# Kernel optimization log

Hardware: AMD Instinct MI355X
Metric: run time of the kernel (lower is better)

The kernel has to match this reference:

```python
import jax, jax.numpy as jnp
import numpy as np

C = 256
NUM_HEADS = 4
GROUPS = 8
EPS = 1e-5


def setup_inputs() -> dict:
    key = jax.random.key(0)
    ks = jax.random.split(key, 8)
    N, H, W = 4, 64, 64
    x = jax.random.normal(ks[0], (N, C, H, W), dtype=jnp.float32)
    mask = jnp.ones((N, 1, H, W), dtype=jnp.float32)
    norm_w = jax.random.normal(ks[1], (C,), dtype=jnp.float32) * 0.02 + 1.0
    norm_b = jax.random.normal(ks[2], (C,), dtype=jnp.float32) * 0.02
    qkv_w = jax.random.normal(ks[3], (3 * C, C), dtype=jnp.float32) * (1.0 / np.sqrt(C))
    qkv_b = jax.random.normal(ks[4], (3 * C,), dtype=jnp.float32) * 0.02
    proj_w = jax.random.normal(ks[5], (C, C), dtype=jnp.float32) * (1.0 / np.sqrt(C))
    proj_b = jax.random.normal(ks[6], (C,), dtype=jnp.float32) * 0.02
    return {"x": x, "mask": mask, "norm_w": norm_w, "norm_b": norm_b,
            "qkv_w": qkv_w, "qkv_b": qkv_b, "proj_w": proj_w, "proj_b": proj_b}


def _group_norm(x, w, b):
    # x: [N, C, H, W]; normalize within GROUPS groups over (C//G, H, W)
    N, Cc, H, W = x.shape
    xg = x.reshape(N, GROUPS, Cc // GROUPS, H, W)
    mean = xg.mean(axis=(2, 3, 4), keepdims=True)
    var = xg.var(axis=(2, 3, 4), keepdims=True)
    xg = (xg - mean) * jax.lax.rsqrt(var + EPS)
    x = xg.reshape(N, Cc, H, W)
    return x * w[None, :, None, None] + b[None, :, None, None]


def reference(x, mask, norm_w, norm_b, qkv_w, qkv_b, proj_w, proj_b):
    N, Cc, H, W = x.shape
    h = NUM_HEADS
    hd = Cc // h  # head dim
    x_norm = _group_norm(x, norm_w, norm_b)
    # 1x1 conv == channel matmul: [N, 3C, H, W]
    qkv = jnp.einsum('nchw,oc->nohw', x_norm, qkv_w) + qkv_b[None, :, None, None]
    q, k, v = jnp.split(qkv, 3, axis=1)
    # n (h c) y x -> n h (y x) c
    def to_heads(t):
        return t.reshape(N, h, hd, H * W).transpose(0, 1, 3, 2)
    q, k, v = to_heads(q), to_heads(k), to_heads(v)
    scale = hd ** (-0.5)
    scores = jnp.einsum('nhic,nhjc->nhij', q, k) * scale  # [N,h,HW,HW]
    probs = jax.nn.softmax(scores, axis=-1)
    out = jnp.einsum('nhij,nhjc->nhic', probs, v)  # [N,h,HW,hd]
    # n h (y x) c -> n (h c) y x
    out = out.transpose(0, 1, 3, 2).reshape(N, Cc, H, W)
    out = jnp.einsum('nchw,oc->nohw', out, proj_w) + proj_b[None, :, None, None]
    y = (x + out) * mask[:, :1, :, :]  # broadcast over C (== repeat)
    return (y, mask)
```

## Files before the change

### kernel.cpp

```cpp
#include <hip/hip_runtime.h>

#define HW 4096
#define EPSV 1e-5f
#define SCL (0.125f * 1.44269504088896341f)

typedef unsigned short u16;
typedef unsigned int u32;
typedef __attribute__((ext_vector_type(8))) short short8;
typedef __attribute__((ext_vector_type(4))) short short4v;
typedef __attribute__((ext_vector_type(4))) float f32x4;

#define MFMA_K32(a, b, c) __builtin_amdgcn_mfma_f32_16x16x32_bf16((a), (b), (c), 0, 0, 0)
#if __has_builtin(__builtin_amdgcn_mfma_f32_16x16x16bf16_1k)
#define MFMA_K16(a, b, c) __builtin_amdgcn_mfma_f32_16x16x16bf16_1k((a), (b), (c), 0, 0, 0)
#elif __has_builtin(__builtin_amdgcn_mfma_f32_16x16x16_bf16)
#define MFMA_K16(a, b, c) __builtin_amdgcn_mfma_f32_16x16x16_bf16((a), (b), (c), 0, 0, 0)
#else
#define MFMA_K16(a, b, c) (c)
#endif

#define GLDS(g, l) __builtin_amdgcn_global_load_lds( \
    (const __attribute__((address_space(1))) u16*)(g), \
    (__attribute__((address_space(3))) u16*)(l), 16, 0, 0)

__device__ __forceinline__ u16 f2b(float f) {
    u32 u = __float_as_uint(f);
    u32 r = (u + 0x7FFFu + ((u >> 16) & 1u)) >> 16;
    return (u16)r;
}

__global__ __launch_bounds__(256) void gn_partial(const float* __restrict__ x, float* __restrict__ ps,
                                                  const float* __restrict__ mask, float* __restrict__ outm) {
    int bid = blockIdx.x;
    int t = threadIdx.x;
    if (bid < 16) {
        ((float4*)outm)[bid * 256 + t] = ((const float4*)mask)[bid * 256 + t];
    }
    const float4* base = (const float4*)x + (size_t)bid * 2048;
    float s = 0.f, sq = 0.f;
    for (int i = t; i < 2048; i += 256) {
        float4 v = base[i];
        s += v.x + v.y + v.z + v.w;
        sq += v.x * v.x + v.y * v.y + v.z * v.z + v.w * v.w;
    }
    __shared__ float rs[256], rq[256];
    rs[t] = s; rq[t] = sq;
    __syncthreads();
    for (int o = 128; o > 0; o >>= 1) {
        if (t < o) { rs[t] += rs[t + o]; rq[t] += rq[t + o]; }
        __syncthreads();
    }
    if (t == 0) { ps[2 * bid] = rs[0]; ps[2 * bid + 1] = rq[0]; }
}

__global__ __launch_bounds__(256) void prep(const float* __restrict__ ps, float* __restrict__ stats,
                                            const float* __restrict__ qkv_w, u16* __restrict__ Wqb,
                                            const float* __restrict__ proj_w, u16* __restrict__ Wpb) {
    int bid = blockIdx.x;
    int t = threadIdx.x;
    if (bid == 0) {
        if (t < 32) {
            float s = 0.f, sq = 0.f;
            for (int i = 0; i < 16; i++) {
                s += ps[2 * (t * 16 + i)];
                sq += ps[2 * (t * 16 + i) + 1];
            }
            float mean = s * (1.f / 131072.f);
            float var = sq * (1.f / 131072.f) - mean * mean;
            stats[t] = mean;
            stats[32 + t] = rsqrtf(var + EPSV);
        }
        return;
    }
    const float* src; u16* dst; int nscaled; int idx;
    if (bid <= 192) { src = qkv_w; dst = Wqb; nscaled = 256; idx = (bid - 1) * 256 + t; }
    else            { src = proj_w; dst = Wpb; nscaled = 0;   idx = (bid - 193) * 256 + t; }
    int row = idx >> 6;
    float sc = (row < nscaled) ? SCL : 1.0f;
    float4 v = *((const float4*)src + idx);
    u32 lo = (u32)f2b(v.x * sc) | ((u32)f2b(v.y * sc) << 16);
    u32 hi = (u32)f2b(v.z * sc) | ((u32)f2b(v.w * sc) << 16);
    uint2 o; o.x = lo; o.y = hi;
    *(uint2*)(dst + (size_t)idx * 4) = o;
}

__global__ __launch_bounds__(256) void gn_apply_t(const float* __restrict__ x, const float* __restrict__ w,
                                                  const float* __restrict__ b, const float* __restrict__ stats,
                                                  u16* __restrict__ xt) {
    __shared__ u16 Tt[64][72];
    int t = threadIdx.x;
    int p0 = blockIdx.x * 64;
    int c0 = blockIdx.y * 64;
    int n = blockIdx.z;
    int pc = (t & 15) * 4;
#pragma unroll
    for (int jj = 0; jj < 4; jj++) {
        int r = (t >> 4) + jj * 16;
        int c = c0 + r;
        int grp = n * 8 + (c >> 5);
        float mean = stats[grp], rstd = stats[32 + grp];
        float a = rstd * w[c];
        float bb = b[c] - mean * a;
        float4 v = *(const float4*)(x + ((size_t)n * 256 + c) * HW + p0 + pc);
        Tt[pc + 0][r] = f2b(v.x * a + bb);
        Tt[pc + 1][r] = f2b(v.y * a + bb);
        Tt[pc + 2][r] = f2b(v.z * a + bb);
        Tt[pc + 3][r] = f2b(v.w * a + bb);
    }
    __syncthreads();
    int p = t >> 2, ck = t & 3;
    short8 s0 = *(const short8*)&Tt[p][ck * 16];
    short8 s1 = *(const short8*)&Tt[p][ck * 16 + 8];
    u16* dst = xt + ((size_t)n * HW + p0 + p) * 256 + c0 + ck * 16;
    *(short8*)dst = s0;
    *(short8*)(dst + 8) = s1;
}

__global__ __launch_bounds__(256) void qkv_mfma(const u16* __restrict__ xt, const u16* __restrict__ Wb,
                                                const float* __restrict__ bq, u16* __restrict__ Qw,
                                                u16* __restrict__ Kw, u16* __restrict__ Vw) {
    __shared__ u16 Xs[64 * 256];
    int t = threadIdx.x;
    int w = t >> 6, lane = t & 63;
    int col = lane & 15, quad = lane >> 4;
    int p0 = blockIdx.x * 64;
    int n = blockIdx.z;

#pragma unroll
    for (int j = 0; j < 8; j++) {
        int rl = j * 2 + (lane >> 5);
        int row = w * 16 + rl;
        int slot = (lane & 31) ^ (rl & 7);
        GLDS(xt + ((size_t)n * HW + p0 + row) * 256 + slot * 8, Xs + (w * 16 + j * 2) * 256);
    }

    const u16* wrow = Wb + (size_t)(w * 16 + col) * 256 + quad * 8;
    short8 A[8];
#pragma unroll
    for (int ks = 0; ks < 8; ks++) A[ks] = *(const short8*)(wrow + ks * 32);

    __syncthreads();

    int c7 = col & 7;
    for (int ot = 0; ot < 12; ot++) {
        int o0 = ot * 64;
        short8 An[8];
        if (ot < 11) {
            const u16* wn = wrow + (size_t)(o0 + 64) * 256;
#pragma unroll
            for (int ks = 0; ks < 8; ks++) An[ks] = *(const short8*)(wn + ks * 32);
        }

        f32x4 C[4];
#pragma unroll
        for (int pb = 0; pb < 4; pb++) C[pb] = (f32x4){0.f, 0.f, 0.f, 0.f};
#pragma unroll
        for (int pb = 0; pb < 4; pb++) {
            const u16* xr = Xs + (pb * 16 + col) * 256;
#pragma unroll
            for (int ks = 0; ks < 8; ks++) {
                int slot = (ks * 4 + quad) ^ c7;
                short8 Bf = *(const short8*)(xr + slot * 8);
                C[pb] = MFMA_K32(A[ks], Bf, C[pb]);
            }
        }

        int type = o0 >> 8;
        int h = (o0 >> 6) & 3;
        int nh = n * 4 + h;
        float sc = (type == 0) ? SCL : 1.0f;
        if (type == 2) {
#pragma unroll
            for (int rg = 0; rg < 4; rg++) {
                int d = w * 16 + quad * 4 + rg;
                float bias = bq[o0 + d];
                u16* vb = Vw + ((size_t)nh * 64 + d) * HW + p0 + col;
#pragma unroll
                for (int pb = 0; pb < 4; pb++)
                    vb[pb * 16] = f2b(C[pb][rg] + bias);
            }
        } else {
            u16* dst = (type == 0 ? Qw : Kw) + ((size_t)nh * HW + p0 + col) * 64 + w * 16 + quad * 4;
            float b0 = sc * bq[o0 + w * 16 + quad * 4 + 0];
            float b1 = sc * bq[o0 + w * 16 + quad * 4 + 1];
            float b2 = sc * bq[o0 + w * 16 + quad * 4 + 2];
            float b3 = sc * bq[o0 + w * 16 + quad * 4 + 3];
#pragma unroll
            for (int pb = 0; pb < 4; pb++) {
                uint2 o;
                o.x = (u32)f2b(C[pb][0] + b0) | ((u32)f2b(C[pb][1] + b1) << 16);
                o.y = (u32)f2b(C[pb][2] + b2) | ((u32)f2b(C[pb][3] + b3) << 16);
                *(uint2*)(dst + (size_t)(pb * 16) * 64) = o;
            }
        }
#pragma unroll
        for (int ks = 0; ks < 8; ks++) A[ks] = An[ks];
    }
}

__global__ __launch_bounds__(512, 4) void flash_mfma(const u16* __restrict__ Qw, const u16* __restrict__ Kw,
                                                     const u16* __restrict__ Vw, u16* __restrict__ attnT) {
    __shared__ u16 Ks[4][64 * 64];
    __shared__ u16 Vts[4][64 * 64];
    int t = threadIdx.x;
    int w = t >> 6, lane = t & 63;
    int half = w >> 2, wl = w & 3;
    int col = lane & 15, quad = lane >> 4;
    int q0 = blockIdx.x * 128;
    int nh = blockIdx.y;

    const u16* qp = Qw + ((size_t)nh * HW + q0 + wl * 32 + col) * 64 + quad * 8;
    short8 qa0 = *(const short8*)qp;
    short8 qa1 = *(const short8*)(qp + 32);
    short8 qc0 = *(const short8*)(qp + 1024);
    short8 qc1 = *(const short8*)(qp + 1024 + 32);

    f32x4 OaA[4], OaB[4];
#pragma unroll
    for (int db = 0; db < 4; db++) {
        OaA[db] = (f32x4){0.f, 0.f, 0.f, 0.f};
        OaB[db] = (f32x4){0.f, 0.f, 0.f, 0.f};
    }
    f32x4 lacA = (f32x4){0.f, 0.f, 0.f, 0.f};
    f32x4 lacB = (f32x4){0.f, 0.f, 0.f, 0.f};

    const u16* kbase = Kw + (size_t)nh * HW * 64;
    const u16* vbase = Vw + (size_t)nh * 64 * HW;
    int lrK = lane >> 3;
    int ccK = lane & 7;
    size_t kSrc = (size_t)(wl * 8 + lrK) * 64 + (ccK ^ lrK) * 8;
    int jbase = half * 2048;

#define STAGE(jt_, b_) do { \
        int j0_ = jbase + (jt_) * 64; \
        _Pragma("unroll") \
        for (int s_ = 0; s_ < 2; s_++) \
            GLDS(kbase + (size_t)j0_ * 64 + kSrc + (size_t)(s_ * 32) * 64, &Ks[half * 2 + (b_)][(wl * 8 + s_ * 32) * 64]); \
        _Pragma("unroll") \
        for (int s_ = 0; s_ < 2; s_++) { \
            int d_ = wl * 8 + s_ * 32 + lrK; \
            GLDS(vbase + (size_t)d_ * HW + j0_ + ((ccK ^ lrK) * 8), &Vts[half * 2 + (b_)][(wl * 8 + s_ * 32) * 64]); \
        } \
    } while (0)

    STAGE(0, 0);
    STAGE(1, 1);

    int c7 = col & 7;
    const short4v ones = {0x3F80, 0x3F80, 0x3F80, 0x3F80};
    for (int jt = 0; jt < 32; jt++) {
        int cur = jt & 1;
        if (jt < 31) { asm volatile("s_waitcnt vmcnt(4)" ::: "memory"); }
        else         { asm volatile("s_waitcnt vmcnt(0)" ::: "memory"); }
        __builtin_amdgcn_s_barrier();

        const u16* KsC = Ks[half * 2 + cur];
        const u16* VtC = Vts[half * 2 + cur];

        f32x4 sA[4], sB[4];
        __builtin_amdgcn_s_setprio(1);
#pragma unroll
        for (int jb = 0; jb < 4; jb++) {
            const u16* kr = KsC + (jb * 16 + col) * 64;
            short8 ka0 = *(const short8*)(kr + ((quad ^ c7) * 8));
            short8 ka1 = *(const short8*)(kr + (((quad + 4) ^ c7) * 8));
            f32x4 a = (f32x4){0.f, 0.f, 0.f, 0.f};
            a = MFMA_K32(ka0, qa0, a);
            a = MFMA_K32(ka1, qa1, a);
            sA[jb] = a;
            f32x4 b = (f32x4){0.f, 0.f, 0.f, 0.f};
            b = MFMA_K32(ka0, qc0, b);
            b = MFMA_K32(ka1, qc1, b);
            sB[jb] = b;
        }
        __builtin_amdgcn_s_setprio(0);

        short4v ptA[4], ptB[4];
#pragma unroll
        for (int jb = 0; jb < 4; jb++) {
            u32 ua[4], ub[4];
#pragma unroll
            for (int rg = 0; rg < 4; rg++) {
                ua[rg] = __float_as_uint(__builtin_amdgcn_exp2f(sA[jb][rg])) + 0x8000u;
                ub[rg] = __float_as_uint(__builtin_amdgcn_exp2f(sB[jb][rg])) + 0x8000u;
            }
            uint2 pa2, pb2;
            pa2.x = __builtin_amdgcn_perm(ua[1], ua[0], 0x07060302u);
            pa2.y = __builtin_amdgcn_perm(ua[3], ua[2], 0x07060302u);
            pb2.x = __builtin_amdgcn_perm(ub[1], ub[0], 0x07060302u);
            pb2.y = __builtin_amdgcn_perm(ub[3], ub[2], 0x07060302u);
            ptA[jb] = __builtin_bit_cast(short4v, pa2);
            ptB[jb] = __builtin_bit_cast(short4v, pb2);
        }

        __builtin_amdgcn_s_setprio(1);
#pragma unroll
        for (int jb = 0; jb < 4; jb++) {
            lacA = MFMA_K16(ones, ptA[jb], lacA);
            lacB = MFMA_K16(ones, ptB[jb], lacB);
        }
#pragma unroll
        for (int db = 0; db < 4; db++) {
            const u16* vr = VtC + (db * 16 + col) * 64;
#pragma unroll
            for (int jb = 0; jb < 4; jb++) {
                int ch = jb * 2 + (quad >> 1);
                short4v va = *(const short4v*)(vr + ((ch ^ c7) * 8) + (quad & 1) * 4);
                OaA[db] = MFMA_K16(va, ptA[jb], OaA[db]);
                OaB[db] = MFMA_K16(va, ptB[jb], OaB[db]);
            }
        }
        __builtin_amdgcn_s_setprio(0);

        __builtin_amdgcn_s_barrier();
        if (jt < 30) STAGE(jt + 2, cur);
    }
#undef STAGE

    float* mO = (float*)&Ks[0][0];
    float* mL = (float*)&Vts[0][0];
    int widx = wl * 64 + lane;
    if (half == 1) {
#pragma unroll
        for (int db = 0; db < 4; db++) {
#pragma unroll
            for (int rg = 0; rg < 4; rg++) {
                mO[(db * 8 + rg) * 256 + widx] = OaA[db][rg];
                mO[(db * 8 + 4 + rg) * 256 + widx] = OaB[db][rg];
            }
        }
        mL[widx] = lacA[0];
        mL[256 + widx] = lacB[0];
    }
    __syncthreads();
    if (half == 0) {
        float lA = lacA[0] + mL[widx];
        float lB = lacB[0] + mL[256 + widx];
        float rlA = 1.0f / lA, rlB = 1.0f / lB;
        u16* abA = attnT + ((size_t)(nh >> 2) * HW + q0 + wl * 32 + col) * 256 + (nh & 3) * 64 + quad * 4;
        u16* abB = abA + 16 * 256;
#pragma unroll
        for (int db = 0; db < 4; db++) {
            float a0 = OaA[db][0] + mO[(db * 8 + 0) * 256 + widx];
            float a1 = OaA[db][1] + mO[(db * 8 + 1) * 256 + widx];
            float a2 = OaA[db][2] + mO[(db * 8 + 2) * 256 + widx];
            float a3 = OaA[db][3] + mO[(db * 8 + 3) * 256 + widx];
            float b0 = OaB[db][0] + mO[(db * 8 + 4) * 256 + widx];
            float b1 = OaB[db][1] + mO[(db * 8 + 5) * 256 + widx];
            float b2 = OaB[db][2] + mO[(db * 8 + 6) * 256 + widx];
            float b3 = OaB[db][3] + mO[(db * 8 + 7) * 256 + widx];
            uint2 oA, oB;
            oA.x = (u32)f2b(a0 * rlA) | ((u32)f2b(a1 * rlA) << 16);
            oA.y = (u32)f2b(a2 * rlA) | ((u32)f2b(a3 * rlA) << 16);
            oB.x = (u32)f2b(b0 * rlB) | ((u32)f2b(b1 * rlB) << 16);
            oB.y = (u32)f2b(b2 * rlB) | ((u32)f2b(b3 * rlB) << 16);
            *(uint2*)(abA + db * 16) = oA;
            *(uint2*)(abB + db * 16) = oB;
        }
    }
}

__global__ __launch_bounds__(256) void proj_mfma(const u16* __restrict__ attnT, const u16* __restrict__ Wpb,
                                                 const float* __restrict__ bp, const float* __restrict__ x,
                                                 const float* __restrict__ mask, float* __restrict__ out) {
    __shared__ u16 Xs[64 * 256];
    int t = threadIdx.x;
    int w = t >> 6, lane = t & 63;
    int col = lane & 15, quad = lane >> 4;
    int p0 = blockIdx.x * 64;
    int n = blockIdx.z;

#pragma unroll
    for (int j = 0; j < 8; j++) {
        int rl = j * 2 + (lane >> 5);
        int row = w * 16 + rl;
        int slot = (lane & 31) ^ (rl & 7);
        GLDS(attnT + ((size_t)n * HW + p0 + row) * 256 + slot * 8, Xs + (w * 16 + j * 2) * 256);
    }

    const u16* wrow = Wpb + (size_t)(w * 16 + col) * 256 + quad * 8;
    short8 A[8];
#pragma unroll
    for (int ks = 0; ks < 8; ks++) A[ks] = *(const short8*)(wrow + ks * 32);

    __syncthreads();

    int c7 = col & 7;
    for (int ot = 0; ot < 4; ot++) {
        int o0 = ot * 64;
        short8 An[8];
        if (ot < 3) {
            const u16* wn = wrow + (size_t)(o0 + 64) * 256;
#pragma unroll
            for (int ks = 0; ks < 8; ks++) An[ks] = *(const short8*)(wn + ks * 32);
        }

        f32x4 C[4];
#pragma unroll
        for (int pb = 0; pb < 4; pb++) C[pb] = (f32x4){0.f, 0.f, 0.f, 0.f};
#pragma unroll
        for (int pb = 0; pb < 4; pb++) {
            const u16* xr = Xs + (pb * 16 + col) * 256;
#pragma unroll
            for (int ks = 0; ks < 8; ks++) {
                int slot = (ks * 4 + quad) ^ c7;
                short8 Bf = *(const short8*)(xr + slot * 8);
                C[pb] = MFMA_K32(A[ks], Bf, C[pb]);
            }
        }

#pragma unroll
        for (int rg = 0; rg < 4; rg++) {
            int o = o0 + w * 16 + quad * 4 + rg;
            float bias = bp[o];
            const float* xb = x + ((size_t)n * 256 + o) * HW + p0 + col;
            float* ob = out + ((size_t)n * 256 + o) * HW + p0 + col;
            const float* mb = mask + (size_t)n * HW + p0 + col;
#pragma unroll
            for (int pb = 0; pb < 4; pb++) {
                float mv = mb[pb * 16];
                ob[pb * 16] = (xb[pb * 16] + C[pb][rg] + bias) * mv;
            }
        }
#pragma unroll
        for (int ks = 0; ks < 8; ks++) A[ks] = An[ks];
    }
}

extern "C" void kernel_launch(void* const* d_in, const int* in_sizes, int n_in,
                              void* d_out, int out_size, void* d_ws, size_t ws_size,
                              hipStream_t stream) {
    const float* x = (const float*)d_in[0];
    const float* mask = (const float*)d_in[1];
    const float* norm_w = (const float*)d_in[2];
    const float* norm_b = (const float*)d_in[3];
    const float* qkv_w = (const float*)d_in[4];
    const float* qkv_b = (const float*)d_in[5];
    const float* proj_w = (const float*)d_in[6];
    const float* proj_b = (const float*)d_in[7];
    float* out = (float*)d_out;

    float* ws = (float*)d_ws;
    float* stats = ws;
    float* pstats = ws + 64;
    u16* xt = (u16*)(ws + 2048);
    u16* Qw = xt + 4194304;
    u16* Kw = Qw + 4194304;
    u16* Vw = Kw + 4194304;
    u16* attnT = Vw + 4194304;
    u16* Wqb = attnT + 4194304;
    u16* Wpb = Wqb + 196608;

    gn_partial<<<512, 256, 0, stream>>>(x, pstats, mask, out + 4194304);
    prep<<<257, 256, 0, stream>>>(pstats, stats, qkv_w, Wqb, proj_w, Wpb);
    gn_apply_t<<<dim3(64, 4, 4), 256, 0, stream>>>(x, norm_w, norm_b, stats, xt);
    qkv_mfma<<<dim3(64, 1, 4), 256, 0, stream>>>(xt, Wqb, qkv_b, Qw, Kw, Vw);
    flash_mfma<<<dim3(32, 16), 512, 0, stream>>>(Qw, Kw, Vw, attnT);
    proj_mfma<<<dim3(64, 1, 4), 256, 0, stream>>>(attnT, Wpb, proj_b, x, mask, out);
}
```

Before: 210.4 us.

## Double query rows per wave in flash attention to increase K/V reuse

Each wave now computes scores and outputs for 64 query rows (four 16-row groups) instead of 32, so every K/V tile staged in LDS and every K/V fragment read is reused across twice as many queries. The grid is halved to 256 blocks and launch bounds are relaxed to allow more registers per thread. The cross-half merge buffer is enlarged to fit the bigger accumulator set. This trades occupancy and register pressure for lower LDS and global traffic per unit of MFMA work.

New measurement: 212.1 us. Within noise of the previous version (+0.8%).

```diff
diff --git a/kernel.cpp b/kernel.cpp
--- a/kernel.cpp
+++ b/kernel.cpp
@@ -198,31 +198,34 @@
     }
 }
 
-__global__ __launch_bounds__(512, 4) void flash_mfma(const u16* __restrict__ Qw, const u16* __restrict__ Kw,
+__global__ __launch_bounds__(512, 2) void flash_mfma(const u16* __restrict__ Qw, const u16* __restrict__ Kw,
                                                      const u16* __restrict__ Vw, u16* __restrict__ attnT) {
-    __shared__ u16 Ks[4][64 * 64];
-    __shared__ u16 Vts[4][64 * 64];
+    __shared__ u16 smem[34816];
+    u16* KsB = smem;
+    u16* VtsB = smem + 16384;
     int t = threadIdx.x;
     int w = t >> 6, lane = t & 63;
     int half = w >> 2, wl = w & 3;
     int col = lane & 15, quad = lane >> 4;
-    int q0 = blockIdx.x * 128;
+    int q0 = blockIdx.x * 256;
     int nh = blockIdx.y;
 
-    const u16* qp = Qw + ((size_t)nh * HW + q0 + wl * 32 + col) * 64 + quad * 8;
-    short8 qa0 = *(const short8*)qp;
-    short8 qa1 = *(const short8*)(qp + 32);
-    short8 qc0 = *(const short8*)(qp + 1024);
-    short8 qc1 = *(const short8*)(qp + 1024 + 32);
-
-    f32x4 OaA[4], OaB[4];
-#pragma unroll
-    for (int db = 0; db < 4; db++) {
-        OaA[db] = (f32x4){0.f, 0.f, 0.f, 0.f};
-        OaB[db] = (f32x4){0.f, 0.f, 0.f, 0.f};
-    }
-    f32x4 lacA = (f32x4){0.f, 0.f, 0.f, 0.f};
-    f32x4 lacB = (f32x4){0.f, 0.f, 0.f, 0.f};
+    const u16* qp = Qw + ((size_t)nh * HW + q0 + wl * 64 + col) * 64 + quad * 8;
+    short8 qf[4][2];
+#pragma unroll
+    for (int g = 0; g < 4; g++) {
+        qf[g][0] = *(const short8*)(qp + g * 1024);
+        qf[g][1] = *(const short8*)(qp + g * 1024 + 32);
+    }
+
+    f32x4 Oa[4][4];
+    f32x4 lac[4];
+#pragma unroll
+    for (int g = 0; g < 4; g++) {
+        lac[g] = (f32x4){0.f, 0.f, 0.f, 0.f};
+#pragma unroll
+        for (int db = 0; db < 4; db++) Oa[g][db] = (f32x4){0.f, 0.f, 0.f, 0.f};
+    }
 
     const u16* kbase = Kw + (size_t)nh * HW * 64;
     const u16* vbase = Vw + (size_t)nh * 64 * HW;
@@ -235,11 +238,11 @@
         int j0_ = jbase + (jt_) * 64; \
         _Pragma("unroll") \
         for (int s_ = 0; s_ < 2; s_++) \
-            GLDS(kbase + (size_t)j0_ * 64 + kSrc + (size_t)(s_ * 32) * 64, &Ks[half * 2 + (b_)][(wl * 8 + s_ * 32) * 64]); \
+            GLDS(kbase + (size_t)j0_ * 64 + kSrc + (size_t)(s_ * 32) * 64, KsB + (half * 2 + (b_)) * 4096 + (wl * 8 + s_ * 32) * 64); \
         _Pragma("unroll") \
         for (int s_ = 0; s_ < 2; s_++) { \
             int d_ = wl * 8 + s_ * 32 + lrK; \
-            GLDS(vbase + (size_t)d_ * HW + j0_ + ((ccK ^ lrK) * 8), &Vts[half * 2 + (b_)][(wl * 8 + s_ * 32) * 64]); \
+            GLDS(vbase + (size_t)d_ * HW + j0_ + ((ccK ^ lrK) * 8), VtsB + (half * 2 + (b_)) * 4096 + (wl * 8 + s_ * 32) * 64); \
         } \
     } while (0)
 
@@ -254,51 +257,48 @@
         else         { asm volatile("s_waitcnt vmcnt(0)" ::: "memory"); }
         __builtin_amdgcn_s_barrier();
 
-        const u16* KsC = Ks[half * 2 + cur];
-        const u16* VtC = Vts[half * 2 + cur];
-
-        f32x4 sA[4], sB[4];
+        const u16* KsC = KsB + (half * 2 + cur) * 4096;
+        const u16* VtC = VtsB + (half * 2 + cur) * 4096;
+
+        f32x4 s[4][4];
         __builtin_amdgcn_s_setprio(1);
 #pragma unroll
         for (int jb = 0; jb < 4; jb++) {
             const u16* kr = KsC + (jb * 16 + col) * 64;
             short8 ka0 = *(const short8*)(kr + ((quad ^ c7) * 8));
             short8 ka1 = *(const short8*)(kr + (((quad + 4) ^ c7) * 8));
-            f32x4 a = (f32x4){0.f, 0.f, 0.f, 0.f};
-            a = MFMA_K32(ka0, qa0, a);
-            a = MFMA_K32(ka1, qa1, a);
-            sA[jb] = a;
-            f32x4 b = (f32x4){0.f, 0.f, 0.f, 0.f};
-            b = MFMA_K32(ka0, qc0, b);
-            b = MFMA_K32(ka1, qc1, b);
-            sB[jb] = b;
+#pragma unroll
+            for (int g = 0; g < 4; g++) {
+                f32x4 a = (f32x4){0.f, 0.f, 0.f, 0.f};
+                a = MFMA_K32(ka0, qf[g][0], a);
+                a = MFMA_K32(ka1, qf[g][1], a);
+                s[jb][g] = a;
+            }
         }
         __builtin_amdgcn_s_setprio(0);
 
-        short4v ptA[4], ptB[4];
+        short4v pt[4][4];
 #pragma unroll
         for (int jb = 0; jb < 4; jb++) {
-            u32 ua[4], ub[4];
-#pragma unroll
-            for (int rg = 0; rg < 4; rg++) {
-                ua[rg] = __float_as_uint(__builtin_amdgcn_exp2f(sA[jb][rg])) + 0x8000u;
-                ub[rg] = __float_as_uint(__builtin_amdgcn_exp2f(sB[jb][rg])) + 0x8000u;
-            }
-            uint2 pa2, pb2;
-            pa2.x = __builtin_amdgcn_perm(ua[1], ua[0], 0x07060302u);
-            pa2.y = __builtin_amdgcn_perm(ua[3], ua[2], 0x07060302u);
-            pb2.x = __builtin_amdgcn_perm(ub[1], ub[0], 0x07060302u);
-            pb2.y = __builtin_amdgcn_perm(ub[3], ub[2], 0x07060302u);
-            ptA[jb] = __builtin_bit_cast(short4v, pa2);
-            ptB[jb] = __builtin_bit_cast(short4v, pb2);
+#pragma unroll
+            for (int g = 0; g < 4; g++) {
+                u32 ua[4];
+#pragma unroll
+                for (int rg = 0; rg < 4; rg++)
+                    ua[rg] = __float_as_uint(__builtin_amdgcn_exp2f(s[jb][g][rg])) + 0x8000u;
+                uint2 p2;
+                p2.x = __builtin_amdgcn_perm(ua[1], ua[0], 0x07060302u);
+                p2.y = __builtin_amdgcn_perm(ua[3], ua[2], 0x07060302u);
+                pt[g][jb] = __builtin_bit_cast(short4v, p2);
+            }
         }
 
         __builtin_amdgcn_s_setprio(1);
 #pragma unroll
-        for (int jb = 0; jb < 4; jb++) {
-            lacA = MFMA_K16(ones, ptA[jb], lacA);
-            lacB = MFMA_K16(ones, ptB[jb], lacB);
-        }
+        for (int g = 0; g < 4; g++)
+#pragma unroll
+            for (int jb = 0; jb < 4; jb++)
+                lac[g] = MFMA_K16(ones, pt[g][jb], lac[g]);
 #pragma unroll
         for (int db = 0; db < 4; db++) {
             const u16* vr = VtC + (db * 16 + col) * 64;
@@ -306,8 +306,9 @@
             for (int jb = 0; jb < 4; jb++) {
                 int ch = jb * 2 + (quad >> 1);
                 short4v va = *(const short4v*)(vr + ((ch ^ c7) * 8) + (quad & 1) * 4);
-                OaA[db] = MFMA_K16(va, ptA[jb], OaA[db]);
-                OaB[db] = MFMA_K16(va, ptB[jb], OaB[db]);
+#pragma unroll
+                for (int g = 0; g < 4; g++)
+                    Oa[g][db] = MFMA_K16(va, pt[g][jb], Oa[g][db]);
             }
         }
         __builtin_amdgcn_s_setprio(0);
@@ -317,45 +318,38 @@
     }
 #undef STAGE
 
-    float* mO = (float*)&Ks[0][0];
-    float* mL = (float*)&Vts[0][0];
+    float* mO = (float*)smem;
+    float* mL = (float*)smem + 16384;
     int widx = wl * 64 + lane;
     if (half == 1) {
 #pragma unroll
-        for (int db = 0; db < 4; db++) {
-#pragma unroll
-            for (int rg = 0; rg < 4; rg++) {
-                mO[(db * 8 + rg) * 256 + widx] = OaA[db][rg];
-                mO[(db * 8 + 4 + rg) * 256 + widx] = OaB[db][rg];
-            }
-        }
-        mL[widx] = lacA[0];
-        mL[256 + widx] = lacB[0];
+        for (int g = 0; g < 4; g++) {
+#pragma unroll
+            for (int db = 0; db < 4; db++)
+#pragma unroll
+                for (int rg = 0; rg < 4; rg++)
+                    mO[((g * 4 + db) * 4 + rg) * 256 + widx] = Oa[g][db][rg];
+            mL[g * 256 + widx] = lac[g][0];
+        }
     }
     __syncthreads();
     if (half == 0) {
-        float lA = lacA[0] + mL[widx];
-        float lB = lacB[0] + mL[256 + widx];
-        float rlA = 1.0f / lA, rlB = 1.0f / lB;
-        u16* abA = attnT + ((size_t)(nh >> 2) * HW + q0 + wl * 32 + col) * 256 + (nh & 3) * 64 + quad * 4;
-        u16* abB = abA + 16 * 256;
-#pragma unroll
-        for (int db = 0; db < 4; db++) {
-            float a0 = OaA[db][0] + mO[(db * 8 + 0) * 256 + widx];
-            float a1 = OaA[db][1] + mO[(db * 8 + 1) * 256 + widx];
-            float a2 = OaA[db][2] + mO[(db * 8 + 2) * 256 + widx];
-            float a3 = OaA[db][3] + mO[(db * 8 + 3) * 256 + widx];
-            float b0 = OaB[db][0] + mO[(db * 8 + 4) * 256 + widx];
-            float b1 = OaB[db][1] + mO[(db * 8 + 5) * 256 + widx];
-            float b2 = OaB[db][2] + mO[(db * 8 + 6) * 256 + widx];
-            float b3 = OaB[db][3] + mO[(db * 8 + 7) * 256 + widx];
-            uint2 oA, oB;
-            oA.x = (u32)f2b(a0 * rlA) | ((u32)f2b(a1 * rlA) << 16);
-            oA.y = (u32)f2b(a2 * rlA) | ((u32)f2b(a3 * rlA) << 16);
-            oB.x = (u32)f2b(b0 * rlB) | ((u32)f2b(b1 * rlB) << 16);
-            oB.y = (u32)f2b(b2 * rlB) | ((u32)f2b(b3 * rlB) << 16);
-            *(uint2*)(abA + db * 16) = oA;
-            *(uint2*)(abB + db * 16) = oB;
+#pragma unroll
+        for (int g = 0; g < 4; g++) {
+            float l = lac[g][0] + mL[g * 256 + widx];
+            float rl = 1.0f / l;
+            u16* ab = attnT + ((size_t)(nh >> 2) * HW + q0 + wl * 64 + g * 16 + col) * 256 + (nh & 3) * 64 + quad * 4;
+#pragma unroll
+            for (int db = 0; db < 4; db++) {
+                float o0v = Oa[g][db][0] + mO[((g * 4 + db) * 4 + 0) * 256 + widx];
+                float o1v = Oa[g][db][1] + mO[((g * 4 + db) * 4 + 1) * 256 + widx];
+                float o2v = Oa[g][db][2] + mO[((g * 4 + db) * 4 + 2) * 256 + widx];
+                float o3v = Oa[g][db][3] + mO[((g * 4 + db) * 4 + 3) * 256 + widx];
+                uint2 o;
+                o.x = (u32)f2b(o0v * rl) | ((u32)f2b(o1v * rl) << 16);
+                o.y = (u32)f2b(o2v * rl) | ((u32)f2b(o3v * rl) << 16);
+                *(uint2*)(ab + db * 16) = o;
+            }
         }
     }
 }
@@ -455,6 +449,6 @@
     prep<<<257, 256, 0, stream>>>(pstats, stats, qkv_w, Wqb, proj_w, Wpb);
     gn_apply_t<<<dim3(64, 4, 4), 256, 0, stream>>>(x, norm_w, norm_b, stats, xt);
     qkv_mfma<<<dim3(64, 1, 4), 256, 0, stream>>>(xt, Wqb, qkv_b, Qw, Kw, Vw);
-    flash_mfma<<<dim3(32, 16), 512, 0, stream>>>(Qw, Kw, Vw, attnT);
+    flash_mfma<<<dim3(16, 16), 512, 0, stream>>>(Qw, Kw, Vw, attnT);
     proj_mfma<<<dim3(64, 1, 4), 256, 0, stream>>>(attnT, Wpb, proj_b, x, mask, out);
 }
```

## Split QKV/proj output channels across grid and compute softmax row sums with VALU

Applied to the files above, without the earlier changes.

The QKV and projection GEMM kernels now split their output channels over a second grid dimension, doubling the block count (512 instead of 256) so more CUs are busy, at the cost of loading the same activation tile twice. In the flash kernel, the row-sum of probabilities is no longer computed with extra MFMAs against a ones vector. It is now accumulated in fp32 on the VALU and reduced with cross-lane shuffles at the end. The bf16 packing switches from manual round-and-perm to the hardware v_cvt_pk_bf16_f32 instruction. The row sum now uses unrounded fp32 values rather than the bf16-rounded probabilities used in P·V, which slightly changes numerics.

New measurement: 199.7 us. -5.1%, faster.

```diff
diff --git a/kernel.cpp b/kernel.cpp
--- a/kernel.cpp
+++ b/kernel.cpp
@@ -124,6 +124,7 @@
     int w = t >> 6, lane = t & 63;
     int col = lane & 15, quad = lane >> 4;
     int p0 = blockIdx.x * 64;
+    int oh = blockIdx.y;
     int n = blockIdx.z;
 
 #pragma unroll
@@ -134,7 +135,7 @@
         GLDS(xt + ((size_t)n * HW + p0 + row) * 256 + slot * 8, Xs + (w * 16 + j * 2) * 256);
     }
 
-    const u16* wrow = Wb + (size_t)(w * 16 + col) * 256 + quad * 8;
+    const u16* wrow = Wb + (size_t)(oh * 384 + w * 16 + col) * 256 + quad * 8;
     short8 A[8];
 #pragma unroll
     for (int ks = 0; ks < 8; ks++) A[ks] = *(const short8*)(wrow + ks * 32);
@@ -142,11 +143,11 @@
     __syncthreads();
 
     int c7 = col & 7;
-    for (int ot = 0; ot < 12; ot++) {
-        int o0 = ot * 64;
+    for (int oi = 0; oi < 6; oi++) {
+        int o0 = oh * 384 + oi * 64;
         short8 An[8];
-        if (ot < 11) {
-            const u16* wn = wrow + (size_t)(o0 + 64) * 256;
+        if (oi < 5) {
+            const u16* wn = wrow + (size_t)(oi + 1) * 64 * 256;
 #pragma unroll
             for (int ks = 0; ks < 8; ks++) An[ks] = *(const short8*)(wn + ks * 32);
         }
@@ -221,8 +222,7 @@
         OaA[db] = (f32x4){0.f, 0.f, 0.f, 0.f};
         OaB[db] = (f32x4){0.f, 0.f, 0.f, 0.f};
     }
-    f32x4 lacA = (f32x4){0.f, 0.f, 0.f, 0.f};
-    f32x4 lacB = (f32x4){0.f, 0.f, 0.f, 0.f};
+    float lacA = 0.f, lacB = 0.f;
 
     const u16* kbase = Kw + (size_t)nh * HW * 64;
     const u16* vbase = Vw + (size_t)nh * 64 * HW;
@@ -247,7 +247,6 @@
     STAGE(1, 1);
 
     int c7 = col & 7;
-    const short4v ones = {0x3F80, 0x3F80, 0x3F80, 0x3F80};
     for (int jt = 0; jt < 32; jt++) {
         int cur = jt & 1;
         if (jt < 31) { asm volatile("s_waitcnt vmcnt(4)" ::: "memory"); }
@@ -278,27 +277,26 @@
         short4v ptA[4], ptB[4];
 #pragma unroll
         for (int jb = 0; jb < 4; jb++) {
-            u32 ua[4], ub[4];
-#pragma unroll
-            for (int rg = 0; rg < 4; rg++) {
-                ua[rg] = __float_as_uint(__builtin_amdgcn_exp2f(sA[jb][rg])) + 0x8000u;
-                ub[rg] = __float_as_uint(__builtin_amdgcn_exp2f(sB[jb][rg])) + 0x8000u;
-            }
+            float ea0 = __builtin_amdgcn_exp2f(sA[jb][0]);
+            float ea1 = __builtin_amdgcn_exp2f(sA[jb][1]);
+            float ea2 = __builtin_amdgcn_exp2f(sA[jb][2]);
+            float ea3 = __builtin_amdgcn_exp2f(sA[jb][3]);
+            float eb0 = __builtin_amdgcn_exp2f(sB[jb][0]);
+            float eb1 = __builtin_amdgcn_exp2f(sB[jb][1]);
+            float eb2 = __builtin_amdgcn_exp2f(sB[jb][2]);
+            float eb3 = __builtin_amdgcn_exp2f(sB[jb][3]);
+            lacA += (ea0 + ea1) + (ea2 + ea3);
+            lacB += (eb0 + eb1) + (eb2 + eb3);
             uint2 pa2, pb2;
-            pa2.x = __builtin_amdgcn_perm(ua[1], ua[0], 0x07060302u);
-            pa2.y = __builtin_amdgcn_perm(ua[3], ua[2], 0x07060302u);
-            pb2.x = __builtin_amdgcn_perm(ub[1], ub[0], 0x07060302u);
-            pb2.y = __builtin_amdgcn_perm(ub[3], ub[2], 0x07060302u);
+            asm("v_cvt_pk_bf16_f32 %0, %1, %2" : "=v"(pa2.x) : "v"(ea0), "v"(ea1));
+            asm("v_cvt_pk_bf16_f32 %0, %1, %2" : "=v"(pa2.y) : "v"(ea2), "v"(ea3));
+            asm("v_cvt_pk_bf16_f32 %0, %1, %2" : "=v"(pb2.x) : "v"(eb0), "v"(eb1));
+            asm("v_cvt_pk_bf16_f32 %0, %1, %2" : "=v"(pb2.y) : "v"(eb2), "v"(eb3));
             ptA[jb] = __builtin_bit_cast(short4v, pa2);
             ptB[jb] = __builtin_bit_cast(short4v, pb2);
         }
 
         __builtin_amdgcn_s_setprio(1);
-#pragma unroll
-        for (int jb = 0; jb < 4; jb++) {
-            lacA = MFMA_K16(ones, ptA[jb], lacA);
-            lacB = MFMA_K16(ones, ptB[jb], lacB);
-        }
 #pragma unroll
         for (int db = 0; db < 4; db++) {
             const u16* vr = VtC + (db * 16 + col) * 64;
@@ -317,6 +315,11 @@
     }
 #undef STAGE
 
+    lacA += __shfl_xor(lacA, 16);
+    lacB += __shfl_xor(lacB, 16);
+    lacA += __shfl_xor(lacA, 32);
+    lacB += __shfl_xor(lacB, 32);
+
     float* mO = (float*)&Ks[0][0];
     float* mL = (float*)&Vts[0][0];
     int widx = wl * 64 + lane;
@@ -329,13 +332,13 @@
                 mO[(db * 8 + 4 + rg) * 256 + widx] = OaB[db][rg];
             }
         }
-        mL[widx] = lacA[0];
-        mL[256 + widx] = lacB[0];
+        mL[widx] = lacA;
+        mL[256 + widx] = lacB;
     }
     __syncthreads();
     if (half == 0) {
-        float lA = lacA[0] + mL[widx];
-        float lB = lacB[0] + mL[256 + widx];
+        float lA = lacA + mL[widx];
+        float lB = lacB + mL[256 + widx];
         float rlA = 1.0f / lA, rlB = 1.0f / lB;
         u16* abA = attnT + ((size_t)(nh >> 2) * HW + q0 + wl * 32 + col) * 256 + (nh & 3) * 64 + quad * 4;
         u16* abB = abA + 16 * 256;
@@ -368,6 +371,7 @@
     int w = t >> 6, lane = t & 63;
     int col = lane & 15, quad = lane >> 4;
     int p0 = blockIdx.x * 64;
+    int oh = blockIdx.y;
     int n = blockIdx.z;
 
 #pragma unroll
@@ -378,7 +382,7 @@
         GLDS(attnT + ((size_t)n * HW + p0 + row) * 256 + slot * 8, Xs + (w * 16 + j * 2) * 256);
     }
 
-    const u16* wrow = Wpb + (size_t)(w * 16 + col) * 256 + quad * 8;
+    const u16* wrow = Wpb + (size_t)(oh * 128 + w * 16 + col) * 256 + quad * 8;
     short8 A[8];
 #pragma unroll
     for (int ks = 0; ks < 8; ks++) A[ks] = *(const short8*)(wrow + ks * 32);
@@ -386,11 +390,11 @@
     __syncthreads();
 
     int c7 = col & 7;
-    for (int ot = 0; ot < 4; ot++) {
-        int o0 = ot * 64;
+    for (int oi = 0; oi < 2; oi++) {
+        int o0 = oh * 128 + oi * 64;
         short8 An[8];
-        if (ot < 3) {
-            const u16* wn = wrow + (size_t)(o0 + 64) * 256;
+        if (oi < 1) {
+            const u16* wn = wrow + (size_t)64 * 256;
 #pragma unroll
             for (int ks = 0; ks < 8; ks++) An[ks] = *(const short8*)(wn + ks * 32);
         }
@@ -454,7 +458,7 @@
     gn_partial<<<512, 256, 0, stream>>>(x, pstats, mask, out + 4194304);
     prep<<<257, 256, 0, stream>>>(pstats, stats, qkv_w, Wqb, proj_w, Wpb);
     gn_apply_t<<<dim3(64, 4, 4), 256, 0, stream>>>(x, norm_w, norm_b, stats, xt);
-    qkv_mfma<<<dim3(64, 1, 4), 256, 0, stream>>>(xt, Wqb, qkv_b, Qw, Kw, Vw);
+    qkv_mfma<<<dim3(64, 2, 4), 256, 0, stream>>>(xt, Wqb, qkv_b, Qw, Kw, Vw);
     flash_mfma<<<dim3(32, 16), 512, 0, stream>>>(Qw, Kw, Vw, attnT);
-    proj_mfma<<<dim3(64, 1, 4), 256, 0, stream>>>(attnT, Wpb, proj_b, x, mask, out);
-}
+    proj_mfma<<<dim3(64, 2, 4), 256, 0, stream>>>(attnT, Wpb, proj_b, x, mask, out);
+}
```
